# Kernel optimization log

Hardware: AMD Instinct MI355X
Metric: run time of the kernel (lower is better)

Reference implementation:

```python
import jax, jax.numpy as jnp
import numpy as np

EPS = 1e-06
BANDWIDTH = 0.1  # scipy minimize x0; frozen on first forward in the original


def _pairwise_sqdist(a, b):
    # a: [B, N, 3], b: [B, M, 3] -> [B, N, M] squared euclidean distances
    a2 = jnp.sum(a * a, axis=-1)  # [B, N]
    b2 = jnp.sum(b * b, axis=-1)  # [B, M]
    ab = jnp.einsum('bnd,bmd->bnm', a, b)  # [B, N, M]
    return jnp.maximum(a2[:, :, None] + b2[:, None, :] - 2.0 * ab, 0.0)


def _compute_density(points, bandwidth):
    # Gaussian KDE over all pairs (self included), normalized by N-1,
    # matching compute_density in the torch source.
    n = points.shape[1]
    sqd = _pairwise_sqdist(points, points)  # [B, N, N]
    kde = jnp.exp(-0.5 * sqd / (bandwidth * bandwidth))
    return jnp.sum(kde, axis=2) / (n - 1)  # [B, N]


def setup_inputs() -> dict:
    key = jax.random.key(0)
    k1, k2 = jax.random.split(key)
    predicted = jax.random.normal(k1, (8, 4096, 3), dtype=jnp.float32)
    ground_truth = jax.random.normal(k2, (8, 4096, 3), dtype=jnp.float32)
    return {
        'predicted': predicted,
        'ground_truth': ground_truth,
        'bandwidth_pred': jnp.float32(BANDWIDTH),
        'bandwidth_gt': jnp.float32(BANDWIDTH),
    }


def reference(predicted, ground_truth, bandwidth_pred, bandwidth_gt):
    # Chamfer distance: per-point squared distance to nearest neighbor in the
    # other cloud (standard ChamferDistance CUDA ext returns squared dists).
    sqd = _pairwise_sqdist(predicted, ground_truth)  # [B, N, M]
    dist_pred_to_gt = jnp.min(sqd, axis=2)  # [B, N]
    dist_gt_to_pred = jnp.min(sqd, axis=1)  # [B, M]

    density_pred = _compute_density(predicted, bandwidth_pred)  # [B, N]
    density_gt = _compute_density(ground_truth, bandwidth_gt)   # [B, M]

    loss_pred_to_gt = jnp.mean(dist_pred_to_gt / (density_pred + EPS))
    loss_gt_to_pred = jnp.mean(dist_gt_to_pred / (density_gt + EPS))
    return loss_pred_to_gt + loss_gt_to_pred
```

## Files before the change

kernel.cpp:

```cpp
#include <hip/hip_runtime.h>


#define NPTS 4096
#define NB   8
#define TS   128
#define TPB  256
#define NT   32
#define BIGF 3.4e38f

#define DENS_BLKS  2048
#define CROSS_BLKS 2048
#define PTSTOT (NB*NPTS)
#define TRIVEC 496

__device__ __forceinline__ void unpack8(const float4* s4, int base,
                                        float (&X)[8], float (&Y)[8], float (&Z)[8])
{
    float4 A = s4[base+0], B = s4[base+1], C = s4[base+2];
    float4 D = s4[base+3], E = s4[base+4], F = s4[base+5];
    X[0]=A.x; Y[0]=A.y; Z[0]=A.z;  X[1]=A.w; Y[1]=B.x; Z[1]=B.y;
    X[2]=B.z; Y[2]=B.w; Z[2]=C.x;  X[3]=C.y; Y[3]=C.z; Z[3]=C.w;
    X[4]=D.x; Y[4]=D.y; Z[4]=D.z;  X[5]=D.w; Y[5]=E.x; Z[5]=E.y;
    X[6]=E.z; Y[6]=E.w; Z[6]=F.x;  X[7]=F.y; Y[7]=F.z; Z[7]=F.w;
}

__global__ __launch_bounds__(TPB) void dacl_pairs(
    const float* __restrict__ pred, const float* __restrict__ gt,
    const float* __restrict__ bwp,  const float* __restrict__ bwg,
    float* __restrict__ minP2Gp,
    float* __restrict__ minG2Pp,
    float* __restrict__ densCol,
    float* __restrict__ densRow)
{
    __shared__ float4 sCol[480];
    __shared__ float4 sRowA[96], sRowB[96];
    __shared__ float  sRed[384];

    const int tid  = threadIdx.x;
    const int ty   = tid & 15;
    const int tx   = tid >> 4;
    const int wave = tid >> 6;
    const int lane = tid & 63;
    const int bid  = blockIdx.x;

    if (bid < DENS_BLKS) {
        const int q  = bid & 7;
        const int u  = (bid >> 3) & 15;
        const int b  = (bid >> 7) & 7;
        const int cl = bid >> 10;

        const float* __restrict__ P = cl ? gt : pred;
        float* __restrict__ dCol = densCol + (size_t)(cl*NB + b) * (TRIVEC*TS);
        float* __restrict__ dRow = densRow + (size_t)(q*2 + cl) * PTSTOT + b*NPTS;
        const float bw = cl ? bwg[0] : bwp[0];
        const float sc = sqrtf(0.5f / (bw*bw*0.6931471805599453f));

        const int n0  = 32 - u;
        const int lo  = (q*33) >> 3;
        const int hi  = ((q+1)*33) >> 3;
        const int nst = hi - lo;
        int nA = n0 - lo; if (nA < 0) nA = 0; if (nA > nst) nA = nst;
        const int tA0 = u + lo;
        const int sB0 = lo > n0 ? lo : n0;
        const int tBs = (31 - u) + (sB0 - n0);

        const float4* cb4 = (const float4*)(P + (size_t)b*NPTS*3);

        if (tid < 96) {
            float4 v = cb4[u*96 + tid];
            v.x*=sc; v.y*=sc; v.z*=sc; v.w*=sc;  sRowA[tid] = v;
        } else if (tid < 192) {
            float4 v = cb4[(31-u)*96 + (tid-96)];
            v.x*=sc; v.y*=sc; v.z*=sc; v.w*=sc;  sRowB[tid-96] = v;
        }
        const int nA96 = nA * 96;
        for (int i = tid; i < nst*96; i += TPB) {
            float4 v = (i < nA96) ? cb4[tA0*96 + i] : cb4[tBs*96 + (i - nA96)];
            v.x*=sc; v.y*=sc; v.z*=sc; v.w*=sc;  sCol[i] = v;
        }
        __syncthreads();

        float rx[8], ry[8], rz[8], nrr[8], racc[8];
        const bool startA = (lo < n0);
        unpack8(startA ? sRowA : sRowB, ty*6, rx, ry, rz);
        #pragma unroll
        for (int r = 0; r < 8; ++r) {
            nrr[r]  = -fmaf(rx[r],rx[r], fmaf(ry[r],ry[r], rz[r]*rz[r]));
            racc[r] = 0.0f;
        }
        int curRT = startA ? u : 31-u;

        auto flushRows = [&](int RTf) {
            float vv[8];
            #pragma unroll
            for (int r = 0; r < 8; ++r) {
                float v = racc[r];
                v += __shfl_xor(v, 16, 64);
                v += __shfl_xor(v, 32, 64);
                vv[r] = v;
            }
            __syncthreads();
            if (wave > 0 && lane < 16) {
                #pragma unroll
                for (int r = 0; r < 8; ++r)
                    sRed[(wave-1)*128 + lane*8 + r] = vv[r];
            }
            __syncthreads();
            if (wave == 0 && lane < 16) {
                #pragma unroll
                for (int r = 0; r < 8; ++r) {
                    const int o = lane*8 + r;
                    dRow[RTf*TS + o] = (vv[r] + sRed[o])
                                     + (sRed[128+o] + sRed[256+o]);
                }
            }
        };

        for (int s = lo; s < hi; ++s) {
            const int t     = s - lo;
            const bool segA = (s < n0);
            const int RT    = segA ? u : 31-u;
            const int TV    = segA ? u + s : (31-u) + (s - n0);

            if (RT != curRT) {
                flushRows(curRT);
                unpack8(sRowB, ty*6, rx, ry, rz);
                #pragma unroll
                for (int r = 0; r < 8; ++r) {
                    nrr[r]  = -fmaf(rx[r],rx[r], fmaf(ry[r],ry[r], rz[r]*rz[r]));
                    racc[r] = 0.0f;
                }
                curRT = RT;
            }

            float cx[8], cy[8], cz[8];
            unpack8(sCol, t*96 + tx*6, cx, cy, cz);

            if (s == 0 || s == n0) {
                #pragma unroll
                for (int c = 0; c < 8; ++c) {
                    const float ax = 2.0f*cx[c], ay = 2.0f*cy[c], az = 2.0f*cz[c];
                    const float ncc = fmaf(-cx[c],cx[c],
                                      fmaf(-cy[c],cy[c], -cz[c]*cz[c]));
                    #pragma unroll
                    for (int r = 0; r < 8; ++r) {
                        float e = fmaf(ax, rx[r], ncc);
                        e = fmaf(ay, ry[r], e);
                        e = fmaf(az, rz[r], e);
                        racc[r] += __builtin_amdgcn_exp2f(e + nrr[r]);
                    }
                }
            } else {
                float cacc[8];
                #pragma unroll
                for (int c = 0; c < 8; ++c) cacc[c] = 0.0f;
                #pragma unroll
                for (int c = 0; c < 8; ++c) {
                    const float ax = 2.0f*cx[c], ay = 2.0f*cy[c], az = 2.0f*cz[c];
                    const float ncc = fmaf(-cx[c],cx[c],
                                      fmaf(-cy[c],cy[c], -cz[c]*cz[c]));
                    #pragma unroll
                    for (int r = 0; r < 8; ++r) {
                        float e = fmaf(ax, rx[r], ncc);
                        e = fmaf(ay, ry[r], e);
                        e = fmaf(az, rz[r], e);
                        const float k = __builtin_amdgcn_exp2f(e + nrr[r]);
                        racc[r] += k;
                        cacc[c] += k;
                    }
                }
                const int triTV = (TV*(TV-1)) >> 1;
                #pragma unroll
                for (int c = 0; c < 8; ++c) {
                    float v = cacc[c];
                    v += __shfl_xor(v, 1, 64);
                    v += __shfl_xor(v, 2, 64);
                    v += __shfl_xor(v, 4, 64);
                    v += __shfl_xor(v, 8, 64);
                    if (ty == 0)
                        dCol[(triTV + RT)*TS + tx*8 + c] = v;
                }
            }
        }
        flushRows(curRT);
    } else {
        const int cb = bid - DENS_BLKS;
        const int b  = cb >> 8;
        const int I  = (cb >> 3) & 31;
        const int ph = cb & 7;

        const float4* pb4 = (const float4*)(pred + (size_t)b*NPTS*3);
        const float4* gb4 = (const float4*)(gt   + (size_t)b*NPTS*3);
        if (tid < 96) sRowA[tid] = pb4[I*96 + tid];
        #pragma unroll
        for (int i = 0; i < 2; ++i) {
            const int o = tid + i*TPB;
            if (o < 384) sCol[o] = gb4[ph*384 + o];
        }
        __syncthreads();

        float rx[8], ry[8], rz[8], rr[8], rmin[8];
        unpack8(sRowA, ty*6, rx, ry, rz);
        #pragma unroll
        for (int r = 0; r < 8; ++r) {
            rr[r]   = fmaf(rx[r],rx[r], fmaf(ry[r],ry[r], rz[r]*rz[r]));
            rmin[r] = BIGF;
        }
        float* __restrict__ mg = minG2Pp + (size_t)I*PTSTOT + b*NPTS;

        for (int t = 0; t < 4; ++t) {
            float cx[8], cy[8], cz[8], cmin[8];
            unpack8(sCol, t*96 + tx*6, cx, cy, cz);
            #pragma unroll
            for (int c = 0; c < 8; ++c) cmin[c] = BIGF;
            #pragma unroll
            for (int c = 0; c < 8; ++c) {
                const float ax = -2.0f*cx[c], ay = -2.0f*cy[c], az = -2.0f*cz[c];
                const float cc = fmaf(cx[c],cx[c], fmaf(cy[c],cy[c], cz[c]*cz[c]));
                #pragma unroll
                for (int r = 0; r < 8; ++r) {
                    float tv = fmaf(ax, rx[r], cc);
                    tv = fmaf(ay, ry[r], tv);
                    tv = fmaf(az, rz[r], tv);
                    rmin[r] = fminf(rmin[r], tv);
                    cmin[c] = fminf(cmin[c], tv + rr[r]);
                }
            }
            #pragma unroll
            for (int c = 0; c < 8; ++c) {
                float v = fmaxf(cmin[c], 0.0f);
                v = fminf(v, __shfl_xor(v, 1, 64));
                v = fminf(v, __shfl_xor(v, 2, 64));
                v = fminf(v, __shfl_xor(v, 4, 64));
                v = fminf(v, __shfl_xor(v, 8, 64));
                if (ty == 0)
                    mg[(ph*4+t)*TS + tx*8 + c] = v;
            }
        }
        float vv[8];
        #pragma unroll
        for (int r = 0; r < 8; ++r) {
            float v = fmaxf(rmin[r] + rr[r], 0.0f);
            v = fminf(v, __shfl_xor(v, 16, 64));
            v = fminf(v, __shfl_xor(v, 32, 64));
            vv[r] = v;
        }
        __syncthreads();
        if (wave > 0 && lane < 16) {
            #pragma unroll
            for (int r = 0; r < 8; ++r) sRed[(wave-1)*128 + lane*8 + r] = vv[r];
        }
        __syncthreads();
        if (wave == 0 && lane < 16) {
            #pragma unroll
            for (int r = 0; r < 8; ++r) {
                const int o = lane*8 + r;
                minP2Gp[(size_t)ph*PTSTOT + b*NPTS + I*TS + o] =
                    fminf(fminf(vv[r], sRed[o]),
                          fminf(sRed[128+o], sRed[256+o]));
            }
        }
    }
}

__global__ __launch_bounds__(256) void dacl_combine(
    const float* __restrict__ minP2Gp, const float* __restrict__ minG2Pp,
    const float* __restrict__ densCol, const float* __restrict__ densRow,
    float* __restrict__ bsum)
{
    const int g   = blockIdx.x * 256 + threadIdx.x;
    const int dir = g >> 15;
    const int idx = g & 32767;
    const int b   = idx >> 12;
    const int pt  = idx & 4095;
    const int T   = pt >> 7;
    const int co  = pt & 127;
    const int cl  = dir;

    float m = BIGF;
    if (dir == 0) {
        #pragma unroll
        for (int s = 0; s < 8; ++s) m = fminf(m, minP2Gp[(size_t)s*PTSTOT + idx]);
    } else {
        #pragma unroll
        for (int s = 0; s < 32; ++s) m = fminf(m, minG2Pp[(size_t)s*PTSTOT + idx]);
    }

    float dn = 0.0f;
    const float* dC = densCol + (size_t)(cl*NB + b)*(TRIVEC*TS)
                      + ((T*(T-1)) >> 1)*TS + co;
    for (int RT = 0; RT < T; ++RT) dn += dC[RT*TS];
    #pragma unroll
    for (int q = 0; q < 8; ++q) {
        const int lo = (q*33) >> 3, hi = ((q+1)*33) >> 3;
        const bool valid = (T < 16) ? (lo < 32 - T) : (hi > T + 1);
        if (valid) dn += densRow[(size_t)(q*2 + cl)*PTSTOT + idx];
    }

    float val = m / (dn * (1.0f/4095.0f) + 1e-6f) * (1.0f/32768.0f);

    #pragma unroll
    for (int off = 32; off; off >>= 1) val += __shfl_down(val, off);
    __shared__ float sm[4];
    const int lane = threadIdx.x & 63, wid = threadIdx.x >> 6;
    if (lane == 0) sm[wid] = val;
    __syncthreads();
    if (threadIdx.x == 0) bsum[blockIdx.x] = (sm[0] + sm[1]) + (sm[2] + sm[3]);
}

__global__ __launch_bounds__(256) void dacl_final(
    const float* __restrict__ bsum, float* __restrict__ out)
{
    float v = bsum[threadIdx.x];
    #pragma unroll
    for (int off = 32; off; off >>= 1) v += __shfl_down(v, off);
    __shared__ float sm[4];
    const int lane = threadIdx.x & 63, wid = threadIdx.x >> 6;
    if (lane == 0) sm[wid] = v;
    __syncthreads();
    if (threadIdx.x == 0) out[0] = (sm[0] + sm[1]) + (sm[2] + sm[3]);
}

extern "C" void kernel_launch(void* const* d_in, const int* in_sizes, int n_in,
                              void* d_out, int out_size, void* d_ws, size_t ws_size,
                              hipStream_t stream)
{
    const float* pred = (const float*)d_in[0];
    const float* gt   = (const float*)d_in[1];
    const float* bwp  = (const float*)d_in[2];
    const float* bwg  = (const float*)d_in[3];

    float* minP2Gp = (float*)d_ws;
    float* minG2Pp = minP2Gp + (size_t)8*PTSTOT;
    float* densCol = minG2Pp + (size_t)32*PTSTOT;
    float* densRow = densCol + (size_t)16*TRIVEC*TS;
    float* bsum    = densRow + (size_t)16*PTSTOT;

    dacl_pairs<<<DENS_BLKS + CROSS_BLKS, TPB, 0, stream>>>(
        pred, gt, bwp, bwg, minP2Gp, minG2Pp, densCol, densRow);
    dacl_combine<<<256, 256, 0, stream>>>(minP2Gp, minG2Pp, densCol, densRow, bsum);
    dacl_final<<<1, 256, 0, stream>>>(bsum, (float*)d_out);
}
```

Before: 89.38 us.

## Rework density triangle work split into per-row-tile chunks and tile chamfer min loop 2x2

Result: no change. 88.86 us (-0.6%).

```diff
diff --git a/kernel.cpp b/kernel.cpp
--- a/kernel.cpp
+++ b/kernel.cpp
@@ -8,7 +8,8 @@
 #define NT   32
 #define BIGF 3.4e38f
 
-#define DENS_BLKS  2048
+#define DCHUNKS    144
+#define DENS_BLKS  (16*DCHUNKS)
 #define CROSS_BLKS 2048
 #define PTSTOT (NB*NPTS)
 #define TRIVEC 496
@@ -32,8 +33,8 @@
     float* __restrict__ densCol,
     float* __restrict__ densRow)
 {
-    __shared__ float4 sCol[480];
-    __shared__ float4 sRowA[96], sRowB[96];
+    __shared__ float4 sCol[384];
+    __shared__ float4 sRow[96];
     __shared__ float  sRed[384];
 
     const int tid  = threadIdx.x;
@@ -44,99 +45,54 @@
     const int bid  = blockIdx.x;
 
     if (bid < DENS_BLKS) {
-        const int q  = bid & 7;
-        const int u  = (bid >> 3) & 15;
-        const int b  = (bid >> 7) & 7;
-        const int cl = bid >> 10;
+        const int cb = bid / DCHUNKS;
+        int rem      = bid - cb * DCHUNKS;
+        const int b  = cb & 7;
+        const int cl = cb >> 3;
+
+        int u = 0;
+        int nc = 8;
+        while (rem >= nc) { rem -= nc; ++u; nc = (35 - u) >> 2; }
+        const int cj = rem;
+        const int js = cj * 4;
+        const int steps = 32 - u;
+        const int je = (js + 4 < steps) ? js + 4 : steps;
+        const int nT = je - js;
 
         const float* __restrict__ P = cl ? gt : pred;
         float* __restrict__ dCol = densCol + (size_t)(cl*NB + b) * (TRIVEC*TS);
-        float* __restrict__ dRow = densRow + (size_t)(q*2 + cl) * PTSTOT + b*NPTS;
+        float* __restrict__ dRow = densRow + (size_t)(cj*2 + cl) * PTSTOT + b*NPTS;
         const float bw = cl ? bwg[0] : bwp[0];
         const float sc = sqrtf(0.5f / (bw*bw*0.6931471805599453f));
 
-        const int n0  = 32 - u;
-        const int lo  = (q*33) >> 3;
-        const int hi  = ((q+1)*33) >> 3;
-        const int nst = hi - lo;
-        int nA = n0 - lo; if (nA < 0) nA = 0; if (nA > nst) nA = nst;
-        const int tA0 = u + lo;
-        const int sB0 = lo > n0 ? lo : n0;
-        const int tBs = (31 - u) + (sB0 - n0);
-
         const float4* cb4 = (const float4*)(P + (size_t)b*NPTS*3);
 
         if (tid < 96) {
             float4 v = cb4[u*96 + tid];
-            v.x*=sc; v.y*=sc; v.z*=sc; v.w*=sc;  sRowA[tid] = v;
-        } else if (tid < 192) {
-            float4 v = cb4[(31-u)*96 + (tid-96)];
-            v.x*=sc; v.y*=sc; v.z*=sc; v.w*=sc;  sRowB[tid-96] = v;
-        }
-        const int nA96 = nA * 96;
-        for (int i = tid; i < nst*96; i += TPB) {
-            float4 v = (i < nA96) ? cb4[tA0*96 + i] : cb4[tBs*96 + (i - nA96)];
+            v.x*=sc; v.y*=sc; v.z*=sc; v.w*=sc;  sRow[tid] = v;
+        }
+        for (int i = tid; i < nT*96; i += TPB) {
+            float4 v = cb4[(u + js)*96 + i];
             v.x*=sc; v.y*=sc; v.z*=sc; v.w*=sc;  sCol[i] = v;
         }
         __syncthreads();
 
         float rx[8], ry[8], rz[8], nrr[8], racc[8];
-        const bool startA = (lo < n0);
-        unpack8(startA ? sRowA : sRowB, ty*6, rx, ry, rz);
+        unpack8(sRow, ty*6, rx, ry, rz);
         #pragma unroll
         for (int r = 0; r < 8; ++r) {
             nrr[r]  = -fmaf(rx[r],rx[r], fmaf(ry[r],ry[r], rz[r]*rz[r]));
             racc[r] = 0.0f;
         }
-        int curRT = startA ? u : 31-u;
-
-        auto flushRows = [&](int RTf) {
-            float vv[8];
-            #pragma unroll
-            for (int r = 0; r < 8; ++r) {
-                float v = racc[r];
-                v += __shfl_xor(v, 16, 64);
-                v += __shfl_xor(v, 32, 64);
-                vv[r] = v;
-            }
-            __syncthreads();
-            if (wave > 0 && lane < 16) {
-                #pragma unroll
-                for (int r = 0; r < 8; ++r)
-                    sRed[(wave-1)*128 + lane*8 + r] = vv[r];
-            }
-            __syncthreads();
-            if (wave == 0 && lane < 16) {
-                #pragma unroll
-                for (int r = 0; r < 8; ++r) {
-                    const int o = lane*8 + r;
-                    dRow[RTf*TS + o] = (vv[r] + sRed[o])
-                                     + (sRed[128+o] + sRed[256+o]);
-                }
-            }
-        };
-
-        for (int s = lo; s < hi; ++s) {
-            const int t     = s - lo;
-            const bool segA = (s < n0);
-            const int RT    = segA ? u : 31-u;
-            const int TV    = segA ? u + s : (31-u) + (s - n0);
-
-            if (RT != curRT) {
-                flushRows(curRT);
-                unpack8(sRowB, ty*6, rx, ry, rz);
-                #pragma unroll
-                for (int r = 0; r < 8; ++r) {
-                    nrr[r]  = -fmaf(rx[r],rx[r], fmaf(ry[r],ry[r], rz[r]*rz[r]));
-                    racc[r] = 0.0f;
-                }
-                curRT = RT;
-            }
+
+        for (int j = js; j < je; ++j) {
+            const int t  = j - js;
+            const int TV = u + j;
 
             float cx[8], cy[8], cz[8];
             unpack8(sCol, t*96 + tx*6, cx, cy, cz);
 
-            if (s == 0 || s == n0) {
+            if (j == 0) {
                 #pragma unroll
                 for (int c = 0; c < 8; ++c) {
                     const float ax = 2.0f*cx[c], ay = 2.0f*cy[c], az = 2.0f*cz[c];
@@ -178,11 +134,35 @@
                     v += __shfl_xor(v, 4, 64);
                     v += __shfl_xor(v, 8, 64);
                     if (ty == 0)
-                        dCol[(triTV + RT)*TS + tx*8 + c] = v;
-                }
-            }
-        }
-        flushRows(curRT);
+                        dCol[(triTV + u)*TS + tx*8 + c] = v;
+                }
+            }
+        }
+        {
+            float vv[8];
+            #pragma unroll
+            for (int r = 0; r < 8; ++r) {
+                float v = racc[r];
+                v += __shfl_xor(v, 16, 64);
+                v += __shfl_xor(v, 32, 64);
+                vv[r] = v;
+            }
+            __syncthreads();
+            if (wave > 0 && lane < 16) {
+                #pragma unroll
+                for (int r = 0; r < 8; ++r)
+                    sRed[(wave-1)*128 + lane*8 + r] = vv[r];
+            }
+            __syncthreads();
+            if (wave == 0 && lane < 16) {
+                #pragma unroll
+                for (int r = 0; r < 8; ++r) {
+                    const int o = lane*8 + r;
+                    dRow[u*TS + o] = (vv[r] + sRed[o])
+                                   + (sRed[128+o] + sRed[256+o]);
+                }
+            }
+        }
     } else {
         const int cb = bid - DENS_BLKS;
         const int b  = cb >> 8;
@@ -191,7 +171,7 @@
 
         const float4* pb4 = (const float4*)(pred + (size_t)b*NPTS*3);
         const float4* gb4 = (const float4*)(gt   + (size_t)b*NPTS*3);
-        if (tid < 96) sRowA[tid] = pb4[I*96 + tid];
+        if (tid < 96) sRow[tid] = pb4[I*96 + tid];
         #pragma unroll
         for (int i = 0; i < 2; ++i) {
             const int o = tid + i*TPB;
@@ -200,7 +180,7 @@
         __syncthreads();
 
         float rx[8], ry[8], rz[8], rr[8], rmin[8];
-        unpack8(sRowA, ty*6, rx, ry, rz);
+        unpack8(sRow, ty*6, rx, ry, rz);
         #pragma unroll
         for (int r = 0; r < 8; ++r) {
             rr[r]   = fmaf(rx[r],rx[r], fmaf(ry[r],ry[r], rz[r]*rz[r]));
@@ -214,21 +194,34 @@
             #pragma unroll
             for (int c = 0; c < 8; ++c) cmin[c] = BIGF;
             #pragma unroll
+            for (int c2 = 0; c2 < 4; ++c2) {
+                const int c0 = 2*c2, c1 = c0 + 1;
+                const float ax0 = -2.0f*cx[c0], ay0 = -2.0f*cy[c0], az0 = -2.0f*cz[c0];
+                const float cc0 = fmaf(cx[c0],cx[c0], fmaf(cy[c0],cy[c0], cz[c0]*cz[c0]));
+                const float ax1 = -2.0f*cx[c1], ay1 = -2.0f*cy[c1], az1 = -2.0f*cz[c1];
+                const float cc1 = fmaf(cx[c1],cx[c1], fmaf(cy[c1],cy[c1], cz[c1]*cz[c1]));
+                #pragma unroll
+                for (int r2 = 0; r2 < 4; ++r2) {
+                    const int r0 = 2*r2, r1 = r0 + 1;
+                    float t00 = fmaf(ax0, rx[r0], cc0);
+                    t00 = fmaf(ay0, ry[r0], t00); t00 = fmaf(az0, rz[r0], t00);
+                    float t01 = fmaf(ax1, rx[r0], cc1);
+                    t01 = fmaf(ay1, ry[r0], t01); t01 = fmaf(az1, rz[r0], t01);
+                    float t10 = fmaf(ax0, rx[r1], cc0);
+                    t10 = fmaf(ay0, ry[r1], t10); t10 = fmaf(az0, rz[r1], t10);
+                    float t11 = fmaf(ax1, rx[r1], cc1);
+                    t11 = fmaf(ay1, ry[r1], t11); t11 = fmaf(az1, rz[r1], t11);
+                    rmin[r0] = fminf(rmin[r0], fminf(t00, t01));
+                    rmin[r1] = fminf(rmin[r1], fminf(t10, t11));
+                    const float d00 = t00 + rr[r0], d01 = t01 + rr[r0];
+                    const float d10 = t10 + rr[r1], d11 = t11 + rr[r1];
+                    cmin[c0] = fminf(cmin[c0], fminf(d00, d10));
+                    cmin[c1] = fminf(cmin[c1], fminf(d01, d11));
+                }
+            }
+            #pragma unroll
             for (int c = 0; c < 8; ++c) {
-                const float ax = -2.0f*cx[c], ay = -2.0f*cy[c], az = -2.0f*cz[c];
-                const float cc = fmaf(cx[c],cx[c], fmaf(cy[c],cy[c], cz[c]*cz[c]));
-                #pragma unroll
-                for (int r = 0; r < 8; ++r) {
-                    float tv = fmaf(ax, rx[r], cc);
-                    tv = fmaf(ay, ry[r], tv);
-                    tv = fmaf(az, rz[r], tv);
-                    rmin[r] = fminf(rmin[r], tv);
-                    cmin[c] = fminf(cmin[c], tv + rr[r]);
-                }
-            }
-            #pragma unroll
-            for (int c = 0; c < 8; ++c) {
-                float v = fmaxf(cmin[c], 0.0f);
+                float v = cmin[c];
                 v = fminf(v, __shfl_xor(v, 1, 64));
                 v = fminf(v, __shfl_xor(v, 2, 64));
                 v = fminf(v, __shfl_xor(v, 4, 64));
@@ -240,7 +233,7 @@
         float vv[8];
         #pragma unroll
         for (int r = 0; r < 8; ++r) {
-            float v = fmaxf(rmin[r] + rr[r], 0.0f);
+            float v = rmin[r] + rr[r];
             v = fminf(v, __shfl_xor(v, 16, 64));
             v = fminf(v, __shfl_xor(v, 32, 64));
             vv[r] = v;
@@ -285,16 +278,16 @@
         #pragma unroll
         for (int s = 0; s < 32; ++s) m = fminf(m, minG2Pp[(size_t)s*PTSTOT + idx]);
     }
+    m = fmaxf(m, 0.0f);
 
     float dn = 0.0f;
     const float* dC = densCol + (size_t)(cl*NB + b)*(TRIVEC*TS)
                       + ((T*(T-1)) >> 1)*TS + co;
     for (int RT = 0; RT < T; ++RT) dn += dC[RT*TS];
+    const int ncj = (35 - T) >> 2;
     #pragma unroll
-    for (int q = 0; q < 8; ++q) {
-        const int lo = (q*33) >> 3, hi = ((q+1)*33) >> 3;
-        const bool valid = (T < 16) ? (lo < 32 - T) : (hi > T + 1);
-        if (valid) dn += densRow[(size_t)(q*2 + cl)*PTSTOT + idx];
+    for (int cj = 0; cj < 8; ++cj) {
+        if (cj < ncj) dn += densRow[(size_t)(cj*2 + cl)*PTSTOT + idx];
     }
 
     float val = m / (dn * (1.0f/4095.0f) + 1e-6f) * (1.0f/32768.0f);
```
